# Kernel tuning notes

Hardware: AMD Instinct MI355X
Metric: run time of the kernel (lower is better)

## Reference

```python
import jax, jax.numpy as jnp
import numpy as np

B, S, D = 2, 2048, 2048
H, KV, HD = 32, 8, 64          # n_heads, n_kv_heads, head_dim
REP = H // KV                  # 4
THETA = 10000.0


def _rotate_half(u):
    h = u.shape[-1] // 2
    return jnp.concatenate([-u[..., h:], u[..., :h]], axis=-1)


def setup_inputs() -> dict:
    key = jax.random.key(0)
    ks = jax.random.split(key, 5)
    x = jax.random.normal(ks[0], (B, S, D), dtype=jnp.float32)
    Wq = jax.random.normal(ks[1], (D, H * HD), dtype=jnp.float32) * 0.02
    Wk = jax.random.normal(ks[2], (D, KV * HD), dtype=jnp.float32) * 0.02
    Wv = jax.random.normal(ks[3], (D, KV * HD), dtype=jnp.float32) * 0.02
    Wo = jax.random.normal(ks[4], (H * HD, D), dtype=jnp.float32) * 0.02
    return {"x": x, "Wq": Wq, "Wk": Wk, "Wv": Wv, "Wo": Wo}


def reference(x, Wq, Wk, Wv, Wo):
    b, s, d = x.shape
    # QKV projections (nn.Linear, no bias)
    q = (x @ Wq).reshape(b, s, H, HD).transpose(0, 2, 1, 3)   # [B,H,S,HD]
    k = (x @ Wk).reshape(b, s, KV, HD).transpose(0, 2, 1, 3)  # [B,KV,S,HD]
    v = (x @ Wv).reshape(b, s, KV, HD).transpose(0, 2, 1, 3)  # [B,KV,S,HD]

    # RoPE (position_offset = 0)
    inv_freq = 1.0 / (THETA ** (jnp.arange(0, HD, 2, dtype=jnp.float32) / HD))
    freqs = jnp.outer(jnp.arange(s, dtype=jnp.float32), inv_freq)  # [S,HD/2]
    emb = jnp.concatenate([freqs, freqs], axis=-1)                  # [S,HD]
    cos, sin = jnp.cos(emb), jnp.sin(emb)
    q = q * cos + _rotate_half(q) * sin
    k = k * cos + _rotate_half(k) * sin

    # Grouped attention: avoid materializing repeated KV tensors.
    qg = q.reshape(b, KV, REP, s, HD)                               # [B,KV,REP,S,HD]
    scale = 1.0 / np.sqrt(HD)
    scores = jnp.einsum('bgrqd,bgkd->bgrqk', qg, k) * scale         # [B,KV,REP,S,S]
    causal = jnp.tril(jnp.ones((s, s), dtype=bool))
    scores = jnp.where(causal, scores, jnp.finfo(jnp.float32).min)
    probs = jax.nn.softmax(scores.astype(jnp.float32), axis=-1).astype(q.dtype)
    out = jnp.einsum('bgrqk,bgkd->bgrqd', probs, v)                 # [B,KV,REP,S,HD]
    out = out.reshape(b, H, s, HD).transpose(0, 2, 1, 3).reshape(b, s, H * HD)
    return out @ Wo                                                  # [B,S,D]
```

## Files before the change

kernel.cpp:

```cpp
#include <hip/hip_runtime.h>
#include <math.h>

typedef __bf16 bf16_t;
typedef bf16_t bf16x8 __attribute__((ext_vector_type(8)));
typedef bf16_t bf16x4 __attribute__((ext_vector_type(4)));
typedef float floatx4 __attribute__((ext_vector_type(4)));
typedef short short4v __attribute__((ext_vector_type(4)));

#define MFMA16(a, b, c) __builtin_amdgcn_mfma_f32_16x16x32_bf16((a), (b), (c), 0, 0, 0)

#if __has_builtin(__builtin_amdgcn_exp2f)
#define PEXP(x) __builtin_amdgcn_exp2f(x)
#define SCORE_SCALE (0.125f * 1.4426950408889634f)
#else
#define PEXP(x) __expf(x)
#define SCORE_SCALE 0.125f
#endif

#if __has_builtin(__builtin_amdgcn_mfma_f32_16x16x16bf16_1k)
#define HAVE_MFMA_K16 1
__device__ __forceinline__ floatx4 mfma_k16(bf16x4 a, bf16x4 b, floatx4 c)
{
    union { bf16x4 v; short4v s; } ua, ub;
    ua.v = a; ub.v = b;
    return __builtin_amdgcn_mfma_f32_16x16x16bf16_1k(ua.s, ub.s, c, 0, 0, 0);
}
#endif

union PU { unsigned u[2]; bf16x4 v; };
union BU { unsigned u[4]; bf16x8 v; };

__device__ __forceinline__ void gld16(const void* g, void* lds)
{
    __builtin_amdgcn_global_load_lds(
        reinterpret_cast<const __attribute__((address_space(1))) void*>(
            reinterpret_cast<uintptr_t>(g)),
        reinterpret_cast<__attribute__((address_space(3))) void*>(
            (unsigned int)reinterpret_cast<uintptr_t>(lds)),
        16, 0, 0);
}

template <int RND>
__device__ __forceinline__ void stageT(
    const bf16_t* __restrict__ g, int K, int r0, int k0,
    bf16_t* lds, int tid, int wave)
{
    #pragma unroll
    for (int i = 0; i < RND; ++i) {
        int c = i * 512 + tid, r = c >> 3, s = c & 7;
        gld16(g + (size_t)(r0 + r) * K + k0 + ((s ^ (r & 7)) << 3),
              lds + (size_t)(i * 512 + wave * 64) * 8);
    }
}

template <typename TC, int BN>
__device__ __forceinline__ void gemm256_body(
    const bf16_t* __restrict__ A, const bf16_t* __restrict__ Bt,
    TC* __restrict__ C, int row0, int col0, int N, int K, bf16_t* smem)
{
    constexpr int NT = BN / 64;
    constexpr int NH = NT / 2;
    constexpr int RB = BN / 64;

    const int tid  = threadIdx.x;
    const int wave = tid >> 6, lane = tid & 63;
    const int quad = lane >> 4, l16 = lane & 15;
    const int wm = (wave >> 2) * 128;
    const int wn = (wave & 3) * (BN / 4);

    bf16_t* As0 = smem;
    bf16_t* As1 = smem + 256 * 64;
    bf16_t* Bs0 = smem + 2 * 256 * 64;
    bf16_t* Bs1 = Bs0 + BN * 64;

    const int ntile = K >> 6;

    floatx4 acc[8][NT] = {};

    stageT<4>(A, K, row0, 0, As0, tid, wave);
    stageT<RB>(Bt, K, col0, 0, Bs0, tid, wave);
    stageT<4>(A, K, row0, 64, As1, tid, wave);

    #pragma unroll 1
    for (int u = 0; u < ntile; ++u) {
        const int d = u & 1;
        bf16_t* Asd = d ? As1 : As0;
        bf16_t* Bsd = d ? Bs1 : Bs0;

        if (u + 1 < ntile)
            __asm__ volatile("s_waitcnt vmcnt(4)" ::: "memory");
        else
            __asm__ volatile("s_waitcnt vmcnt(0)" ::: "memory");
        __builtin_amdgcn_s_barrier();
        __asm__ volatile("" ::: "memory");

        if (u + 1 < ntile)
            stageT<RB>(Bt, K, col0, (u + 1) << 6, d ? Bs0 : Bs1, tid, wave);

        bf16x8 af[8][2], bfr[NH][2];
        #pragma unroll
        for (int mt = 0; mt < 8; ++mt)
            #pragma unroll
            for (int kh = 0; kh < 2; ++kh) {
                int ar = wm + mt * 16 + l16;
                af[mt][kh] = *(const bf16x8*)&Asd[ar * 64 +
                    (((kh * 4 + quad) ^ (ar & 7)) << 3)];
            }
        #pragma unroll
        for (int j = 0; j < NH; ++j)
            #pragma unroll
            for (int kh = 0; kh < 2; ++kh) {
                int br = wn + j * 16 + l16;
                bfr[j][kh] = *(const bf16x8*)&Bsd[br * 64 +
                    (((kh * 4 + quad) ^ (br & 7)) << 3)];
            }

        __builtin_amdgcn_s_setprio(1);
        #pragma unroll
        for (int kh = 0; kh < 2; ++kh)
            #pragma unroll
            for (int mt = 0; mt < 8; ++mt)
                #pragma unroll
                for (int j = 0; j < NH; ++j)
                    acc[mt][j] = MFMA16(af[mt][kh], bfr[j][kh], acc[mt][j]);
        __builtin_amdgcn_s_setprio(0);

        __asm__ volatile("s_waitcnt lgkmcnt(0)" ::: "memory");
        __builtin_amdgcn_s_barrier();
        __asm__ volatile("" ::: "memory");

        if (u + 2 < ntile)
            stageT<4>(A, K, row0, (u + 2) << 6, Asd, tid, wave);

        bf16x8 bf1[NH][2];
        #pragma unroll
        for (int j = 0; j < NH; ++j)
            #pragma unroll
            for (int kh = 0; kh < 2; ++kh) {
                int br = wn + (NH + j) * 16 + l16;
                bf1[j][kh] = *(const bf16x8*)&Bsd[br * 64 +
                    (((kh * 4 + quad) ^ (br & 7)) << 3)];
            }

        __builtin_amdgcn_s_setprio(1);
        #pragma unroll
        for (int kh = 0; kh < 2; ++kh)
            #pragma unroll
            for (int mt = 0; mt < 8; ++mt)
                #pragma unroll
                for (int j = 0; j < NH; ++j)
                    acc[mt][NH + j] = MFMA16(af[mt][kh], bf1[j][kh],
                                             acc[mt][NH + j]);
        __builtin_amdgcn_s_setprio(0);
    }

    #pragma unroll
    for (int mt = 0; mt < 8; ++mt)
        #pragma unroll
        for (int nt = 0; nt < NT; ++nt)
            #pragma unroll
            for (int r = 0; r < 4; ++r)
                C[(size_t)(row0 + wm + mt * 16 + quad * 4 + r) * N
                  + col0 + wn + nt * 16 + l16] = (TC)acc[mt][nt][r];
}

__global__ __launch_bounds__(512, 2) void gemm256_qkv(
    const bf16_t* __restrict__ A, const bf16_t* __restrict__ BtQ,
    const bf16_t* __restrict__ BtK, const bf16_t* __restrict__ BtV,
    bf16_t* __restrict__ CQ, bf16_t* __restrict__ CK, bf16_t* __restrict__ CV)
{
    extern __shared__ __align__(16) bf16_t smem[];
    const int x = blockIdx.x;
    const bf16_t* Bt; bf16_t* C; int N, col0;
    if (x < 8)       { Bt = BtQ; C = CQ; N = 2048; col0 = x * 256; }
    else if (x < 10) { Bt = BtK; C = CK; N = 512;  col0 = (x - 8) * 256; }
    else             { Bt = BtV; C = CV; N = 512;  col0 = (x - 10) * 256; }
    gemm256_body<bf16_t, 256>(A, Bt, C, blockIdx.y * 256, col0, N, 2048, smem);
}

__global__ __launch_bounds__(512, 2) void gemm256_out(
    const bf16_t* __restrict__ A, const bf16_t* __restrict__ Bt,
    float* __restrict__ C)
{
    extern __shared__ __align__(16) bf16_t smem[];
    gemm256_body<float, 128>(A, Bt, C, blockIdx.y * 256, blockIdx.x * 128,
                             2048, 2048, smem);
}

__device__ __forceinline__ void transpose_body(
    const float* __restrict__ W, bf16_t* __restrict__ Wt, int K, int N,
    int bx, int by, float (*t)[33], int tid)
{
    int tx = tid & 31, ty = tid >> 5;
    #pragma unroll
    for (int i = 0; i < 32; i += 8)
        t[ty + i][tx] = W[(size_t)(by + ty + i) * N + bx + tx];
    __syncthreads();
    #pragma unroll
    for (int i = 0; i < 32; i += 8)
        Wt[(size_t)(bx + ty + i) * K + by + tx] = (bf16_t)t[tx][ty + i];
}

__global__ __launch_bounds__(256) void prep_all(
    const float* __restrict__ x, const float* __restrict__ Wq,
    const float* __restrict__ Wk, const float* __restrict__ Wv,
    bf16_t* __restrict__ xb, bf16_t* __restrict__ WqT,
    bf16_t* __restrict__ WkT, bf16_t* __restrict__ WvT)
{
    __shared__ float t[32][33];
    const int blk = blockIdx.x, tid = threadIdx.x;
    if (blk < 8192) {
        int i = blk * 256 + tid;
        float4 f = ((const float4*)x)[i];
        bf16x4 v = {(bf16_t)f.x, (bf16_t)f.y, (bf16_t)f.z, (bf16_t)f.w};
        ((bf16x4*)xb)[i] = v;
    } else if (blk < 12288) {
        int r = blk - 8192;
        transpose_body(Wq, WqT, 2048, 2048, (r & 63) * 32, (r >> 6) * 32, t, tid);
    } else if (blk < 13312) {
        int r = blk - 12288;
        transpose_body(Wk, WkT, 2048, 512, (r & 15) * 32, (r >> 4) * 32, t, tid);
    } else {
        int r = blk - 13312;
        transpose_body(Wv, WvT, 2048, 512, (r & 15) * 32, (r >> 4) * 32, t, tid);
    }
}

__global__ __launch_bounds__(256) void mid_all(
    bf16_t* __restrict__ Kw, const bf16_t* __restrict__ Vw,
    bf16_t* __restrict__ VtG, const float* __restrict__ Wo,
    bf16_t* __restrict__ WoT)
{
    __shared__ float tf[32][33];
    __shared__ bf16_t tb[32][34];
    const int blk = blockIdx.x, tid = threadIdx.x;
    if (blk < 4096) {
        int idx = blk * 256 + tid;
        int i   = idx & 31;
        int h   = (idx >> 5) & 7;
        int row = idx >> 8;
        int pos = row & 2047;
        float invf = powf(10000.0f, -(float)i / 32.0f);
        float sv, cv;
        sincosf((float)pos * invf, &sv, &cv);
        size_t base = (size_t)row * 512 + (size_t)h * 64 + i;
        float a  = (float)Kw[base];
        float b2 = (float)Kw[base + 32];
        Kw[base]      = (bf16_t)(a * cv - b2 * sv);
        Kw[base + 32] = (bf16_t)(b2 * cv + a * sv);
    } else if (blk < 6144) {
        int r  = blk - 4096;
        int bz = r >> 10, r2 = r & 1023;
        int bx = (r2 & 15) * 32, by = (r2 >> 4) * 32;
        int tx = tid & 31, ty = tid >> 5;
        #pragma unroll
        for (int i = 0; i < 32; i += 8)
            tb[ty + i][tx] = Vw[((size_t)bz * 2048 + by + ty + i) * 512 + bx + tx];
        __syncthreads();
        #pragma unroll
        for (int i = 0; i < 32; i += 8)
            VtG[((size_t)bz * 512 + bx + ty + i) * 2048 + by + tx] = tb[tx][ty + i];
    } else {
        int r = blk - 6144;
        transpose_body(Wo, WoT, 2048, 2048, (r & 63) * 32, (r >> 6) * 32, tf, tid);
    }
}

__global__ __launch_bounds__(256) void gqa_attn(
    const bf16_t* __restrict__ Q, const bf16_t* __restrict__ Kc,
    const bf16_t* __restrict__ Vt, bf16_t* __restrict__ AO)
{
    __shared__ alignas(16) bf16_t Ks[2][64 * 64];
    __shared__ alignas(16) bf16_t Vs[2][64 * 64];

    const int x = blockIdx.x, h = blockIdx.y, b = blockIdx.z, g = h >> 2;
    const int tid  = threadIdx.x;
    const int wave = tid >> 6, lane = tid & 63;
    const int quad = lane >> 4, l16 = lane & 15;

    #pragma unroll 1
    for (int t = 0; t < 2; ++t) {
        const int qt = t ? x : (31 - x);
        const int qb = qt * 64 + wave * 16;

        bf16x8 qf[2];
        {
            int qrow = qb + l16;
            const bf16_t* qp = Q + (size_t)(b * 2048 + qrow) * 2048 + h * 64 + quad * 8;
            bf16x8 lo = *(const bf16x8*)qp;
            bf16x8 hi = *(const bf16x8*)(qp + 32);
            #pragma unroll
            for (int j = 0; j < 8; ++j) {
                int d = quad * 8 + j;
                float invf = powf(10000.0f, -(float)d / 32.0f);
                float sv, cv;
                sincosf((float)qrow * invf, &sv, &cv);
                float a = (float)lo[j], c2 = (float)hi[j];
                qf[0][j] = (bf16_t)((a * cv - c2 * sv) * SCORE_SCALE);
                qf[1][j] = (bf16_t)((c2 * cv + a * sv) * SCORE_SCALE);
            }
        }

        floatx4 o[4] = {};
        floatx4 ls4 = {};

        const int ktmax = qt;

        __asm__ volatile("s_waitcnt lgkmcnt(0)" ::: "memory");
        __builtin_amdgcn_s_barrier();
        #pragma unroll
        for (int i = 0; i < 2; ++i) {
            int c = i * 256 + tid;
            int r = c >> 3, s = c & 7;
            int sw = (s ^ (r & 7)) << 3;
            gld16(Kc + (size_t)(b * 2048 + r) * 512 + g * 64 + sw,
                  &Ks[0][(i * 256 + wave * 64) * 8]);
            gld16(Vt + (size_t)(b * 512 + g * 64 + r) * 2048 + sw,
                  &Vs[0][(i * 256 + wave * 64) * 8]);
        }

        #pragma unroll 1
        for (int kt = 0; kt <= ktmax; ++kt) {
            const int cur = kt & 1;
            if (kt < ktmax) {
                const int kn = kt + 1;
                #pragma unroll
                for (int i = 0; i < 2; ++i) {
                    int c = i * 256 + tid;
                    int r = c >> 3, s = c & 7;
                    int sw = (s ^ (r & 7)) << 3;
                    gld16(Kc + (size_t)(b * 2048 + kn * 64 + r) * 512 + g * 64 + sw,
                          &Ks[cur ^ 1][(i * 256 + wave * 64) * 8]);
                    gld16(Vt + (size_t)(b * 512 + g * 64 + r) * 2048 + kn * 64 + sw,
                          &Vs[cur ^ 1][(i * 256 + wave * 64) * 8]);
                }
                __asm__ volatile("s_waitcnt vmcnt(4)" ::: "memory");
            } else {
                __asm__ volatile("s_waitcnt vmcnt(0)" ::: "memory");
            }
            __builtin_amdgcn_s_barrier();

            floatx4 st[4] = {};
            #pragma unroll
            for (int nt = 0; nt < 4; ++nt) {
                int kr = nt * 16 + l16;
                bf16x8 kf0 = *(const bf16x8*)&Ks[cur][kr * 64 + ((quad ^ (kr & 7)) << 3)];
                bf16x8 kf1 = *(const bf16x8*)&Ks[cur][kr * 64 + (((4 + quad) ^ (kr & 7)) << 3)];
                st[nt] = MFMA16(kf0, qf[0], st[nt]);
                st[nt] = MFMA16(kf1, qf[1], st[nt]);
            }

            PU pk[4];
            {
                const bool diag = (kt == qt);
                const int qa = qb + l16;
                #pragma unroll
                for (int nt = 0; nt < 4; ++nt) {
                    float pv[4];
                    #pragma unroll
                    for (int r = 0; r < 4; ++r) {
                        float e = PEXP(st[nt][r]);
                        if (diag) {
                            int ka = kt * 64 + nt * 16 + quad * 4 + r;
                            if (ka > qa) e = 0.f;
                        }
                        ls4[r] += e;
                        pv[r] = e;
                    }
                    pk[nt].v = bf16x4{(bf16_t)pv[0], (bf16_t)pv[1],
                                      (bf16_t)pv[2], (bf16_t)pv[3]};
                }
            }

#ifdef HAVE_MFMA_K16
            #pragma unroll
            for (int nt = 0; nt < 4; ++nt)
                #pragma unroll
                for (int dt = 0; dt < 4; ++dt) {
                    int vr = dt * 16 + l16;
                    int slot = ((nt << 1) | (quad >> 1)) ^ (vr & 7);
                    bf16x4 va = *(const bf16x4*)&Vs[cur][vr * 64 + (slot << 3)
                                                         + ((quad & 1) << 2)];
                    o[dt] = mfma_k16(va, pk[nt].v, o[dt]);
                }
#else
            #pragma unroll
            for (int H = 0; H < 2; ++H) {
                BU bfv;
                #pragma unroll
                for (int j = 0; j < 4; ++j) {
                    int srcl = (((quad & 1) << 1) + (j >> 1)) * 16 + l16;
                    unsigned a0 = (unsigned)__shfl((int)pk[2 * H].u[j & 1], srcl, 64);
                    unsigned a1 = (unsigned)__shfl((int)pk[2 * H + 1].u[j & 1], srcl, 64);
                    bfv.u[j] = (quad >> 1) ? a1 : a0;
                }
                #pragma unroll
                for (int dt = 0; dt < 4; ++dt) {
                    int vr = dt * 16 + l16;
                    bf16x8 va = *(const bf16x8*)&Vs[cur][vr * 64
                                  + ((((H << 2) | quad) ^ (vr & 7)) << 3)];
                    o[dt] = MFMA16(va, bfv.v, o[dt]);
                }
            }
#endif
            __asm__ volatile("s_waitcnt lgkmcnt(0)" ::: "memory");
            __builtin_amdgcn_s_barrier();
        }

        float l = ls4[0] + ls4[1] + ls4[2] + ls4[3];
        l += __shfl_xor(l, 16, 64);
        l += __shfl_xor(l, 32, 64);
        float rc = 1.0f / l;
        #pragma unroll
        for (int dt = 0; dt < 4; ++dt) {
            bf16x4 ov = {(bf16_t)(o[dt][0] * rc), (bf16_t)(o[dt][1] * rc),
                         (bf16_t)(o[dt][2] * rc), (bf16_t)(o[dt][3] * rc)};
            *(bf16x4*)&AO[(size_t)(b * 2048 + qb + l16) * 2048
                          + h * 64 + dt * 16 + quad * 4] = ov;
        }
    }
}

extern "C" void kernel_launch(void* const* d_in, const int* in_sizes, int n_in,
                              void* d_out, int out_size, void* d_ws, size_t ws_size,
                              hipStream_t stream)
{
    const float* x  = (const float*)d_in[0];
    const float* Wq = (const float*)d_in[1];
    const float* Wk = (const float*)d_in[2];
    const float* Wv = (const float*)d_in[3];
    const float* Wo = (const float*)d_in[4];
    float* out = (float*)d_out;

    const size_t MB = 1024 * 1024;
    char* ws = (char*)d_ws;
    bf16_t* xb_AO = (bf16_t*)(ws);
    bf16_t* WqoT  = (bf16_t*)(ws + 16 * MB);
    bf16_t* WkT   = (bf16_t*)(ws + 24 * MB);
    bf16_t* WvT   = (bf16_t*)(ws + 26 * MB);
    bf16_t* Qw    = (bf16_t*)(ws + 28 * MB);
    bf16_t* Kw    = (bf16_t*)(ws + 44 * MB);
    bf16_t* Vw    = (bf16_t*)(ws + 48 * MB);
    bf16_t* VtG   = (bf16_t*)(ws + 52 * MB);

    static bool s_attr = false;
    if (!s_attr) {
        hipFuncSetAttribute(reinterpret_cast<const void*>(gemm256_qkv),
                            hipFuncAttributeMaxDynamicSharedMemorySize, 131072);
        hipFuncSetAttribute(reinterpret_cast<const void*>(gemm256_out),
                            hipFuncAttributeMaxDynamicSharedMemorySize, 98304);
        s_attr = true;
    }

    prep_all<<<14336, 256, 0, stream>>>(x, Wq, Wk, Wv, xb_AO, WqoT, WkT, WvT);

    gemm256_qkv<<<dim3(12, 16), 512, 131072, stream>>>(
        xb_AO, WqoT, WkT, WvT, Qw, Kw, Vw);

    mid_all<<<10240, 256, 0, stream>>>(Kw, Vw, VtG, Wo, WqoT);

    gqa_attn<<<dim3(16, 32, 2), 256, 0, stream>>>(Qw, Kw, VtG, xb_AO);

    gemm256_out<<<dim3(16, 16), 512, 98304, stream>>>(xb_AO, WqoT, out);
}
```

Baseline: 306.1 us.

## Share K/V tiles across the four heads of a GQA group in attention

Attention blocks are remapped so each block handles one KV group, with each of its four waves handling one query head of that group over a 32-row query tile split into two 16-row MFMA subtiles. Each K/V tile loaded into LDS is therefore reused by four heads instead of being loaded separately per head, which cuts global and LDS traffic per unit of work. Each wave now keeps twice the accumulators and Q fragments, raising register pressure. A launch-bounds hint of two blocks per CU is added, and the causal diagonal now covers 64-key tiles with 32-row query tiles, so some masked work is still computed.

```diff
diff --git a/kernel.cpp b/kernel.cpp
--- a/kernel.cpp
+++ b/kernel.cpp
@@ -266,26 +266,31 @@
     }
 }
 
-__global__ __launch_bounds__(256) void gqa_attn(
+__global__ __launch_bounds__(256, 2) void gqa_attn(
     const bf16_t* __restrict__ Q, const bf16_t* __restrict__ Kc,
     const bf16_t* __restrict__ Vt, bf16_t* __restrict__ AO)
 {
     __shared__ alignas(16) bf16_t Ks[2][64 * 64];
     __shared__ alignas(16) bf16_t Vs[2][64 * 64];
 
-    const int x = blockIdx.x, h = blockIdx.y, b = blockIdx.z, g = h >> 2;
+    const int x = blockIdx.x, g = blockIdx.y, b = blockIdx.z;
     const int tid  = threadIdx.x;
     const int wave = tid >> 6, lane = tid & 63;
     const int quad = lane >> 4, l16 = lane & 15;
+    const int h = g * 4 + wave;
 
     #pragma unroll 1
     for (int t = 0; t < 2; ++t) {
-        const int qt = t ? x : (31 - x);
-        const int qb = qt * 64 + wave * 16;
-
-        bf16x8 qf[2];
-        {
-            int qrow = qb + l16;
+        const int qt = t ? x : (63 - x);
+        const int q0 = qt * 32;
+        int qb[2];
+        qb[0] = q0;
+        qb[1] = q0 + 16;
+
+        bf16x8 qf[2][2];
+        #pragma unroll
+        for (int mt = 0; mt < 2; ++mt) {
+            int qrow = qb[mt] + l16;
             const bf16_t* qp = Q + (size_t)(b * 2048 + qrow) * 2048 + h * 64 + quad * 8;
             bf16x8 lo = *(const bf16x8*)qp;
             bf16x8 hi = *(const bf16x8*)(qp + 32);
@@ -296,15 +301,15 @@
                 float sv, cv;
                 sincosf((float)qrow * invf, &sv, &cv);
                 float a = (float)lo[j], c2 = (float)hi[j];
-                qf[0][j] = (bf16_t)((a * cv - c2 * sv) * SCORE_SCALE);
-                qf[1][j] = (bf16_t)((c2 * cv + a * sv) * SCORE_SCALE);
+                qf[mt][0][j] = (bf16_t)((a * cv - c2 * sv) * SCORE_SCALE);
+                qf[mt][1][j] = (bf16_t)((c2 * cv + a * sv) * SCORE_SCALE);
             }
         }
 
-        floatx4 o[4] = {};
-        floatx4 ls4 = {};
-
-        const int ktmax = qt;
+        floatx4 o[2][4] = {};
+        floatx4 ls4[2] = {};
+
+        const int ktmax = qt >> 1;
 
         __asm__ volatile("s_waitcnt lgkmcnt(0)" ::: "memory");
         __builtin_amdgcn_s_barrier();
@@ -340,35 +345,38 @@
             }
             __builtin_amdgcn_s_barrier();
 
-            floatx4 st[4] = {};
+            floatx4 st[2][4] = {};
             #pragma unroll
             for (int nt = 0; nt < 4; ++nt) {
                 int kr = nt * 16 + l16;
                 bf16x8 kf0 = *(const bf16x8*)&Ks[cur][kr * 64 + ((quad ^ (kr & 7)) << 3)];
                 bf16x8 kf1 = *(const bf16x8*)&Ks[cur][kr * 64 + (((4 + quad) ^ (kr & 7)) << 3)];
-                st[nt] = MFMA16(kf0, qf[0], st[nt]);
-                st[nt] = MFMA16(kf1, qf[1], st[nt]);
-            }
-
-            PU pk[4];
-            {
-                const bool diag = (kt == qt);
-                const int qa = qb + l16;
+                st[0][nt] = MFMA16(kf0, qf[0][0], st[0][nt]);
+                st[0][nt] = MFMA16(kf1, qf[0][1], st[0][nt]);
+                st[1][nt] = MFMA16(kf0, qf[1][0], st[1][nt]);
+                st[1][nt] = MFMA16(kf1, qf[1][1], st[1][nt]);
+            }
+
+            PU pk[2][4];
+            const bool diag = (kt == ktmax);
+            #pragma unroll
+            for (int mt = 0; mt < 2; ++mt) {
+                const int qa = qb[mt] + l16;
                 #pragma unroll
                 for (int nt = 0; nt < 4; ++nt) {
                     float pv[4];
                     #pragma unroll
                     for (int r = 0; r < 4; ++r) {
-                        float e = PEXP(st[nt][r]);
+                        float e = PEXP(st[mt][nt][r]);
                         if (diag) {
                             int ka = kt * 64 + nt * 16 + quad * 4 + r;
                             if (ka > qa) e = 0.f;
                         }
-                        ls4[r] += e;
+                        ls4[mt][r] += e;
                         pv[r] = e;
                     }
-                    pk[nt].v = bf16x4{(bf16_t)pv[0], (bf16_t)pv[1],
-                                      (bf16_t)pv[2], (bf16_t)pv[3]};
+                    pk[mt][nt].v = bf16x4{(bf16_t)pv[0], (bf16_t)pv[1],
+                                          (bf16_t)pv[2], (bf16_t)pv[3]};
                 }
             }
 
@@ -381,25 +389,30 @@
                     int slot = ((nt << 1) | (quad >> 1)) ^ (vr & 7);
                     bf16x4 va = *(const bf16x4*)&Vs[cur][vr * 64 + (slot << 3)
                                                          + ((quad & 1) << 2)];
-                    o[dt] = mfma_k16(va, pk[nt].v, o[dt]);
+                    o[0][dt] = mfma_k16(va, pk[0][nt].v, o[0][dt]);
+                    o[1][dt] = mfma_k16(va, pk[1][nt].v, o[1][dt]);
                 }
 #else
             #pragma unroll
             for (int H = 0; H < 2; ++H) {
-                BU bfv;
-                #pragma unroll
-                for (int j = 0; j < 4; ++j) {
-                    int srcl = (((quad & 1) << 1) + (j >> 1)) * 16 + l16;
-                    unsigned a0 = (unsigned)__shfl((int)pk[2 * H].u[j & 1], srcl, 64);
-                    unsigned a1 = (unsigned)__shfl((int)pk[2 * H + 1].u[j & 1], srcl, 64);
-                    bfv.u[j] = (quad >> 1) ? a1 : a0;
+                BU bfv[2];
+                #pragma unroll
+                for (int mt = 0; mt < 2; ++mt) {
+                    #pragma unroll
+                    for (int j = 0; j < 4; ++j) {
+                        int srcl = (((quad & 1) << 1) + (j >> 1)) * 16 + l16;
+                        unsigned a0 = (unsigned)__shfl((int)pk[mt][2 * H].u[j & 1], srcl, 64);
+                        unsigned a1 = (unsigned)__shfl((int)pk[mt][2 * H + 1].u[j & 1], srcl, 64);
+                        bfv[mt].u[j] = (quad >> 1) ? a1 : a0;
+                    }
                 }
                 #pragma unroll
                 for (int dt = 0; dt < 4; ++dt) {
                     int vr = dt * 16 + l16;
                     bf16x8 va = *(const bf16x8*)&Vs[cur][vr * 64
                                   + ((((H << 2) | quad) ^ (vr & 7)) << 3)];
-                    o[dt] = MFMA16(va, bfv.v, o[dt]);
+                    o[0][dt] = MFMA16(va, bfv[0].v, o[0][dt]);
+                    o[1][dt] = MFMA16(va, bfv[1].v, o[1][dt]);
                 }
             }
 #endif
@@ -407,16 +420,19 @@
             __builtin_amdgcn_s_barrier();
         }
 
-        float l = ls4[0] + ls4[1] + ls4[2] + ls4[3];
-        l += __shfl_xor(l, 16, 64);
-        l += __shfl_xor(l, 32, 64);
-        float rc = 1.0f / l;
-        #pragma unroll
-        for (int dt = 0; dt < 4; ++dt) {
-            bf16x4 ov = {(bf16_t)(o[dt][0] * rc), (bf16_t)(o[dt][1] * rc),
-                         (bf16_t)(o[dt][2] * rc), (bf16_t)(o[dt][3] * rc)};
-            *(bf16x4*)&AO[(size_t)(b * 2048 + qb + l16) * 2048
-                          + h * 64 + dt * 16 + quad * 4] = ov;
+        #pragma unroll
+        for (int mt = 0; mt < 2; ++mt) {
+            float l = ls4[mt][0] + ls4[mt][1] + ls4[mt][2] + ls4[mt][3];
+            l += __shfl_xor(l, 16, 64);
+            l += __shfl_xor(l, 32, 64);
+            float rc = 1.0f / l;
+            #pragma unroll
+            for (int dt = 0; dt < 4; ++dt) {
+                bf16x4 ov = {(bf16_t)(o[mt][dt][0] * rc), (bf16_t)(o[mt][dt][1] * rc),
+                             (bf16_t)(o[mt][dt][2] * rc), (bf16_t)(o[mt][dt][3] * rc)};
+                *(bf16x4*)&AO[(size_t)(b * 2048 + qb[mt] + l16) * 2048
+                              + h * 64 + dt * 16 + quad * 4] = ov;
+            }
         }
     }
 }
@@ -459,7 +475,7 @@
 
     mid_all<<<10240, 256, 0, stream>>>(Kw, Vw, VtG, Wo, WqoT);
 
-    gqa_attn<<<dim3(16, 32, 2), 256, 0, stream>>>(Qw, Kw, VtG, xb_AO);
+    gqa_attn<<<dim3(32, 8, 2), 256, 0, stream>>>(Qw, Kw, VtG, xb_AO);
 
     gemm256_out<<<dim3(16, 16), 512, 98304, stream>>>(xb_AO, WqoT, out);
 }
```

Result: faster. 285.2 us (-6.8%).
